# Performance work log

Hardware: AMD Instinct MI355X
Metric: run time of the kernel (lower is better)

## Reference

```python
import jax, jax.numpy as jnp
import numpy as np

N = 100000      # nodes
E = 1600000     # edges (avg degree 16)
F_IN = 64       # graph_input_dim
HID = 64        # gcn_out_dims (constant)
NG = 128        # number of graphs in batch
GF = 32         # global_input_dim
L1, L2, OUT = 256, 128, 1


def _glorot(k, fan_in, fan_out):
    s = 1.0 / np.sqrt(fan_in)
    return jax.random.uniform(k, (fan_in, fan_out), jnp.float32, -s, s)


def setup_inputs() -> dict:
    key = jax.random.key(0)
    ks = jax.random.split(key, 20)
    x = jax.random.normal(ks[0], (N, F_IN), jnp.float32)
    edge_index = jax.random.randint(ks[1], (2, E), 0, N, jnp.int64)
    # every graph gets a contiguous, non-empty slice of nodes (sorted batch ids)
    batch = (jnp.arange(N, dtype=jnp.int64) * NG) // N
    global_features = jax.random.normal(ks[2], (NG, GF), jnp.float32)
    dims = [F_IN, HID, HID, HID]
    inp = {"x": x, "global_features": global_features}
    for i in range(3):
        inp[f"conv_w{i+1}"] = _glorot(ks[3 + i], dims[i], dims[i + 1])
        inp[f"conv_b{i+1}"] = jnp.zeros((dims[i + 1],), jnp.float32)
    inp["fc_w1"] = _glorot(ks[8], HID * 2 + GF, L1)
    inp["fc_b1"] = jnp.zeros((L1,), jnp.float32)
    inp["fc_w2"] = _glorot(ks[9], L1, L2)
    inp["fc_b2"] = jnp.zeros((L2,), jnp.float32)
    inp["out_w"] = _glorot(ks[10], L2, OUT)
    inp["out_b"] = jnp.zeros((OUT,), jnp.float32)
    inp["edge_index"] = edge_index
    inp["batch"] = batch
    return inp


def _gcn_conv(x, src, dst, w, b, n):
    """PyG GCNConv: x' = D^-1/2 (A + I) D^-1/2 (x W) + b."""
    h = x @ w  # [n, out]
    loop = jnp.arange(n, dtype=src.dtype)
    s = jnp.concatenate([src, loop])
    d = jnp.concatenate([dst, loop])
    deg = jax.ops.segment_sum(jnp.ones(s.shape, h.dtype), d, num_segments=n)
    dinv = jnp.where(deg > 0, jax.lax.rsqrt(deg), 0.0)
    norm = dinv[s] * dinv[d]  # [E+n]
    out = jax.ops.segment_sum(h[s] * norm[:, None], d, num_segments=n)
    return out + b


def _forward(x, global_features, conv_w1, conv_b1, conv_w2, conv_b2,
             conv_w3, conv_b3, fc_w1, fc_b1, fc_w2, fc_b2, out_w, out_b,
             edge_index, batch):
    src, dst = edge_index[0], edge_index[1]
    n = x.shape[0]
    ng = global_features.shape[0]
    for w, b in ((conv_w1, conv_b1), (conv_w2, conv_b2), (conv_w3, conv_b3)):
        x = jax.nn.leaky_relu(_gcn_conv(x, src, dst, w, b, n))
    counts = jax.ops.segment_sum(jnp.ones((n,), x.dtype), batch, num_segments=ng)
    mean_pool = jax.ops.segment_sum(x, batch, num_segments=ng) / counts[:, None]
    max_pool = jax.ops.segment_max(x, batch, num_segments=ng)
    h = jnp.concatenate([mean_pool, max_pool, global_features], axis=1)
    h = jax.nn.leaky_relu(h @ fc_w1 + fc_b1)
    h = jax.nn.leaky_relu(h @ fc_w2 + fc_b2)
    return h @ out_w + out_b


def reference(x, global_features, conv_w1, conv_b1, conv_w2, conv_b2,
              conv_w3, conv_b3, fc_w1, fc_b1, fc_w2, fc_b2, out_w, out_b,
              edge_index, batch):
    return _forward(x, global_features, conv_w1, conv_b1, conv_w2, conv_b2,
                    conv_w3, conv_b3, fc_w1, fc_b1, fc_w2, fc_b2, out_w, out_b,
                    edge_index, batch)
```

## Files before the change

### kernel.cpp

```cpp
#include <hip/hip_runtime.h>
#include <hip/hip_fp16.h>
#include <stdint.h>

#define LRELU(x) ((x) > 0.0f ? (x) : 0.01f * (x))

struct h4 { __half2 a, b; };
struct h8 { __half2 a, b, c, d; };

#define EPB 2048
#define PARTS 16


__global__ __launch_bounds__(256) void hist1_kernel(const int* __restrict__ dst,
                                                    int* __restrict__ bhist,
                                                    int nblk, int E, int nbk) {
    __shared__ int h[512];
    int blk = blockIdx.x, t = threadIdx.x;
    for (int i = t; i < nbk; i += 256) h[i] = 0;
    __syncthreads();
    #pragma unroll
    for (int k = 0; k < EPB / 1024; ++k) {
        int i4 = blk * (EPB / 4) + k * 256 + t;
        int e = i4 * 4;
        if (e + 3 < E) {
            int4 d = ((const int4*)dst)[i4];
            atomicAdd(&h[d.x >> 8], 1);
            atomicAdd(&h[d.y >> 8], 1);
            atomicAdd(&h[d.z >> 8], 1);
            atomicAdd(&h[d.w >> 8], 1);
        } else {
            for (int j = e; j < E; ++j) atomicAdd(&h[dst[j] >> 8], 1);
        }
    }
    __syncthreads();
    for (int i = t; i < nbk; i += 256) bhist[i * nblk + blk] = h[i];
}

__global__ __launch_bounds__(256) void scanb_kernel(int* __restrict__ bhist,
                                                    int* __restrict__ btot, int nblk) {
    __shared__ int s[256];
    __shared__ int carry;
    int b = blockIdx.x, t = threadIdx.x;
    if (t == 0) carry = 0;
    __syncthreads();
    for (int c0 = 0; c0 < nblk; c0 += 256) {
        int idx = c0 + t;
        int v = (idx < nblk) ? bhist[b * nblk + idx] : 0;
        s[t] = v;
        __syncthreads();
        for (int off = 1; off < 256; off <<= 1) {
            int a = (t >= off) ? s[t - off] : 0;
            __syncthreads();
            s[t] += a;
            __syncthreads();
        }
        if (idx < nblk) bhist[b * nblk + idx] = s[t] - v + carry;
        __syncthreads();
        if (t == 255) carry += s[255];
        __syncthreads();
    }
    if (t == 0) btot[b] = carry;
}

__global__ void bbase_kernel(const int* __restrict__ btot, int* __restrict__ bbase,
                             int nbk, int E) {
    __shared__ int s[512];
    int t = threadIdx.x;
    int v = (t < nbk) ? btot[t] : 0;
    s[t] = v;
    __syncthreads();
    for (int off = 1; off < 512; off <<= 1) {
        int a = (t >= off) ? s[t - off] : 0;
        __syncthreads();
        s[t] += a;
        __syncthreads();
    }
    if (t < nbk) bbase[t] = s[t] - v;
    if (t == 0) bbase[nbk] = E;
}

__global__ __launch_bounds__(256) void place_kernel(const int* __restrict__ src,
                                                    const int* __restrict__ dst,
                                                    const int* __restrict__ bbase,
                                                    const int* __restrict__ bhist,
                                                    unsigned* __restrict__ bedge,
                                                    int nblk, int E, int nbk) {
    __shared__ int cur[512];
    int blk = blockIdx.x, t = threadIdx.x;
    for (int i = t; i < nbk; i += 256) cur[i] = bbase[i] + bhist[i * nblk + blk];
    __syncthreads();
    #pragma unroll
    for (int k = 0; k < EPB / 1024; ++k) {
        int i4 = blk * (EPB / 4) + k * 256 + t;
        int e = i4 * 4;
        if (e + 3 < E) {
            int4 s4 = ((const int4*)src)[i4];
            int4 d4 = ((const int4*)dst)[i4];
            int p0 = atomicAdd(&cur[d4.x >> 8], 1);
            int p1 = atomicAdd(&cur[d4.y >> 8], 1);
            int p2 = atomicAdd(&cur[d4.z >> 8], 1);
            int p3 = atomicAdd(&cur[d4.w >> 8], 1);
            bedge[p0] = ((unsigned)s4.x << 8) | (unsigned)(d4.x & 255);
            bedge[p1] = ((unsigned)s4.y << 8) | (unsigned)(d4.y & 255);
            bedge[p2] = ((unsigned)s4.z << 8) | (unsigned)(d4.z & 255);
            bedge[p3] = ((unsigned)s4.w << 8) | (unsigned)(d4.w & 255);
        } else {
            for (int j = e; j < E; ++j) {
                int d = dst[j];
                int pos = atomicAdd(&cur[d >> 8], 1);
                bedge[pos] = ((unsigned)src[j] << 8) | (unsigned)(d & 255);
            }
        }
    }
}

__global__ __launch_bounds__(256) void csr_kernel(const unsigned* __restrict__ bedge,
                                                  const int* __restrict__ bbase,
                                                  int* __restrict__ row_ptr,
                                                  float* __restrict__ dinv,
                                                  int* __restrict__ csr_src,
                                                  int N, int E, int nbk) {
    __shared__ int cnt[256];
    __shared__ int s[256];
    __shared__ int cur[256];
    int b = blockIdx.x, t = threadIdx.x;
    int node0 = b << 8;
    int beg = bbase[b], end = bbase[b + 1];
    cnt[t] = 0;
    __syncthreads();
    for (int i = beg + t; i < end; i += 256) atomicAdd(&cnt[bedge[i] & 255u], 1);
    __syncthreads();
    int c = cnt[t];
    s[t] = c;
    __syncthreads();
    for (int off = 1; off < 256; off <<= 1) {
        int a = (t >= off) ? s[t - off] : 0;
        __syncthreads();
        s[t] += a;
        __syncthreads();
    }
    int rp = beg + s[t] - c;
    int node = node0 + t;
    if (node < N) {
        row_ptr[node] = rp;
        dinv[node] = rsqrtf((float)c + 1.0f);
    }
    cur[t] = rp;
    if (b == nbk - 1 && t == 0) row_ptr[N] = E;
    __syncthreads();
    for (int i = beg + t; i < end; i += 256) {
        unsigned u = bedge[i];
        int pos = atomicAdd(&cur[u & 255u], 1);
        csr_src[pos] = (int)(u >> 8);
    }
}


__global__ __launch_bounds__(256) void gemm_f_kernel(const float* __restrict__ X,
                                                     const float* __restrict__ W,
                                                     const float* __restrict__ dinv,
                                                     __half* __restrict__ H, int N) {
    __shared__ float xl[64 * 66];
    __shared__ float wl[64 * 64];
    int tid = threadIdx.x;
    int base = blockIdx.x * 64;
    #pragma unroll
    for (int i = 0; i < 16; ++i) wl[i * 256 + tid] = W[i * 256 + tid];
    #pragma unroll
    for (int i = 0; i < 16; ++i) {
        int idx = i * 256 + tid;
        int r = idx >> 6, c = idx & 63;
        int gr = base + r;
        xl[r * 66 + c] = (gr < N) ? X[gr * 64 + c] : 0.0f;
    }
    __syncthreads();
    int grp = tid >> 4;
    int f0 = (tid & 15) * 4;
    int n0 = grp * 4;
    float acc[4][4] = {};
    #pragma unroll 4
    for (int k = 0; k < 64; ++k) {
        float4 wv = *(const float4*)&wl[k * 64 + f0];
        #pragma unroll
        for (int j = 0; j < 4; ++j) {
            float xv = xl[(n0 + j) * 66 + k];
            acc[j][0] += xv * wv.x;
            acc[j][1] += xv * wv.y;
            acc[j][2] += xv * wv.z;
            acc[j][3] += xv * wv.w;
        }
    }
    #pragma unroll
    for (int j = 0; j < 4; ++j) {
        int gr = base + n0 + j;
        if (gr < N) {
            float dv = dinv[gr];
            h4 o;
            o.a = __floats2half2_rn(acc[j][0] * dv, acc[j][1] * dv);
            o.b = __floats2half2_rn(acc[j][2] * dv, acc[j][3] * dv);
            *(h4*)&H[gr * 64 + f0] = o;
        }
    }
}

__global__ __launch_bounds__(256) void gemm_h_kernel(const __half* __restrict__ X,
                                                     const float* __restrict__ W,
                                                     const float* __restrict__ dinv,
                                                     __half* __restrict__ H, int N) {
    __shared__ float xl[64 * 66];
    __shared__ float wl[64 * 64];
    int tid = threadIdx.x;
    int base = blockIdx.x * 64;
    #pragma unroll
    for (int i = 0; i < 16; ++i) wl[i * 256 + tid] = W[i * 256 + tid];
    #pragma unroll
    for (int i = 0; i < 2; ++i) {
        int u = i * 256 + tid;
        int r = u >> 3;
        int c8 = (u & 7) * 8;
        int gr = base + r;
        float* xp = &xl[r * 66 + c8];
        if (gr < N) {
            h8 v = *(const h8*)&X[(size_t)gr * 64 + c8];
            float2 p;
            p = __half22float2(v.a); xp[0] = p.x; xp[1] = p.y;
            p = __half22float2(v.b); xp[2] = p.x; xp[3] = p.y;
            p = __half22float2(v.c); xp[4] = p.x; xp[5] = p.y;
            p = __half22float2(v.d); xp[6] = p.x; xp[7] = p.y;
        } else {
            #pragma unroll
            for (int j = 0; j < 8; ++j) xp[j] = 0.0f;
        }
    }
    __syncthreads();
    int grp = tid >> 4;
    int f0 = (tid & 15) * 4;
    int n0 = grp * 4;
    float acc[4][4] = {};
    #pragma unroll 4
    for (int k = 0; k < 64; ++k) {
        float4 wv = *(const float4*)&wl[k * 64 + f0];
        #pragma unroll
        for (int j = 0; j < 4; ++j) {
            float xv = xl[(n0 + j) * 66 + k];
            acc[j][0] += xv * wv.x;
            acc[j][1] += xv * wv.y;
            acc[j][2] += xv * wv.z;
            acc[j][3] += xv * wv.w;
        }
    }
    #pragma unroll
    for (int j = 0; j < 4; ++j) {
        int gr = base + n0 + j;
        if (gr < N) {
            float dv = dinv[gr];
            h4 o;
            o.a = __floats2half2_rn(acc[j][0] * dv, acc[j][1] * dv);
            o.b = __floats2half2_rn(acc[j][2] * dv, acc[j][3] * dv);
            *(h4*)&H[gr * 64 + f0] = o;
        }
    }
}

#define ACC8(vv, c0, c1, c2, c3, c4, c5, c6, c7)                                \
    { float2 p;                                                                 \
      p = __half22float2((vv).a); c0 += p.x; c1 += p.y;                         \
      p = __half22float2((vv).b); c2 += p.x; c3 += p.y;                         \
      p = __half22float2((vv).c); c4 += p.x; c5 += p.y;                         \
      p = __half22float2((vv).d); c6 += p.x; c7 += p.y; }

__global__ __launch_bounds__(256) void agg_kernel(const __half* __restrict__ H,
                                                  const int* __restrict__ rp,
                                                  const int* __restrict__ csrc,
                                                  const float* __restrict__ dinv,
                                                  const float* __restrict__ bias,
                                                  __half* __restrict__ Y, int N) {
    int w = (blockIdx.x * blockDim.x + threadIdx.x) >> 6;
    int nA = w << 1;
    if (nA >= N) return;
    int nB = nA + 1;
    bool hasB = nB < N;
    int l = threadIdx.x & 63;
    int slot = l >> 3;
    int fo = (l & 7) << 3;
    int endA = rp[nA + 1];
    int eA = rp[nA] + slot;
    int endB = hasB ? rp[nB + 1] : 0;
    int eB = hasB ? (rp[nB] + slot) : 0;
    float a0=0,a1=0,a2=0,a3=0,a4=0,a5=0,a6=0,a7=0;
    float b0=0,b1=0,b2=0,b3=0,b4=0,b5=0,b6=0,b7=0;
    while (eA + 8 < endA && eB + 8 < endB) {
        int sA0 = csrc[eA], sA1 = csrc[eA + 8];
        int sB0 = csrc[eB], sB1 = csrc[eB + 8];
        h8 vA0 = *(const h8*)&H[(size_t)sA0 * 64 + fo];
        h8 vA1 = *(const h8*)&H[(size_t)sA1 * 64 + fo];
        h8 vB0 = *(const h8*)&H[(size_t)sB0 * 64 + fo];
        h8 vB1 = *(const h8*)&H[(size_t)sB1 * 64 + fo];
        ACC8(vA0, a0,a1,a2,a3,a4,a5,a6,a7);
        ACC8(vA1, a0,a1,a2,a3,a4,a5,a6,a7);
        ACC8(vB0, b0,b1,b2,b3,b4,b5,b6,b7);
        ACC8(vB1, b0,b1,b2,b3,b4,b5,b6,b7);
        eA += 16; eB += 16;
    }
    while (eA + 8 < endA) {
        int s0 = csrc[eA], s1 = csrc[eA + 8];
        h8 v0 = *(const h8*)&H[(size_t)s0 * 64 + fo];
        h8 v1 = *(const h8*)&H[(size_t)s1 * 64 + fo];
        ACC8(v0, a0,a1,a2,a3,a4,a5,a6,a7);
        ACC8(v1, a0,a1,a2,a3,a4,a5,a6,a7);
        eA += 16;
    }
    while (eB + 8 < endB) {
        int s0 = csrc[eB], s1 = csrc[eB + 8];
        h8 v0 = *(const h8*)&H[(size_t)s0 * 64 + fo];
        h8 v1 = *(const h8*)&H[(size_t)s1 * 64 + fo];
        ACC8(v0, b0,b1,b2,b3,b4,b5,b6,b7);
        ACC8(v1, b0,b1,b2,b3,b4,b5,b6,b7);
        eB += 16;
    }
    if (eA < endA) {
        h8 v0 = *(const h8*)&H[(size_t)csrc[eA] * 64 + fo];
        ACC8(v0, a0,a1,a2,a3,a4,a5,a6,a7);
    }
    if (eB < endB) {
        h8 v0 = *(const h8*)&H[(size_t)csrc[eB] * 64 + fo];
        ACC8(v0, b0,b1,b2,b3,b4,b5,b6,b7);
    }
    #pragma unroll
    for (int m = 8; m <= 32; m <<= 1) {
        a0 += __shfl_xor(a0, m); a1 += __shfl_xor(a1, m);
        a2 += __shfl_xor(a2, m); a3 += __shfl_xor(a3, m);
        a4 += __shfl_xor(a4, m); a5 += __shfl_xor(a5, m);
        a6 += __shfl_xor(a6, m); a7 += __shfl_xor(a7, m);
        b0 += __shfl_xor(b0, m); b1 += __shfl_xor(b1, m);
        b2 += __shfl_xor(b2, m); b3 += __shfl_xor(b3, m);
        b4 += __shfl_xor(b4, m); b5 += __shfl_xor(b5, m);
        b6 += __shfl_xor(b6, m); b7 += __shfl_xor(b7, m);
    }
    if (l < 8) {
        float4 bv0 = *(const float4*)&bias[fo];
        float4 bv1 = *(const float4*)&bias[fo + 4];
        {
            h8 hs = *(const h8*)&H[(size_t)nA * 64 + fo];
            float2 s0 = __half22float2(hs.a), s1 = __half22float2(hs.b);
            float2 s2 = __half22float2(hs.c), s3 = __half22float2(hs.d);
            float dv = dinv[nA];
            float o0 = LRELU(dv * (a0 + s0.x) + bv0.x);
            float o1 = LRELU(dv * (a1 + s0.y) + bv0.y);
            float o2 = LRELU(dv * (a2 + s1.x) + bv0.z);
            float o3 = LRELU(dv * (a3 + s1.y) + bv0.w);
            float o4 = LRELU(dv * (a4 + s2.x) + bv1.x);
            float o5 = LRELU(dv * (a5 + s2.y) + bv1.y);
            float o6 = LRELU(dv * (a6 + s3.x) + bv1.z);
            float o7 = LRELU(dv * (a7 + s3.y) + bv1.w);
            h8 o;
            o.a = __floats2half2_rn(o0, o1);
            o.b = __floats2half2_rn(o2, o3);
            o.c = __floats2half2_rn(o4, o5);
            o.d = __floats2half2_rn(o6, o7);
            *(h8*)&Y[(size_t)nA * 64 + fo] = o;
        }
        if (hasB) {
            h8 hs = *(const h8*)&H[(size_t)nB * 64 + fo];
            float2 s0 = __half22float2(hs.a), s1 = __half22float2(hs.b);
            float2 s2 = __half22float2(hs.c), s3 = __half22float2(hs.d);
            float dv = dinv[nB];
            float o0 = LRELU(dv * (b0 + s0.x) + bv0.x);
            float o1 = LRELU(dv * (b1 + s0.y) + bv0.y);
            float o2 = LRELU(dv * (b2 + s1.x) + bv0.z);
            float o3 = LRELU(dv * (b3 + s1.y) + bv0.w);
            float o4 = LRELU(dv * (b4 + s2.x) + bv1.x);
            float o5 = LRELU(dv * (b5 + s2.y) + bv1.y);
            float o6 = LRELU(dv * (b6 + s3.x) + bv1.z);
            float o7 = LRELU(dv * (b7 + s3.y) + bv1.w);
            h8 o;
            o.a = __floats2half2_rn(o0, o1);
            o.b = __floats2half2_rn(o2, o3);
            o.c = __floats2half2_rn(o4, o5);
            o.d = __floats2half2_rn(o6, o7);
            *(h8*)&Y[(size_t)nB * 64 + fo] = o;
        }
    }
}


__global__ void bounds_kernel(const int* __restrict__ batch, int* __restrict__ gstart,
                              int N, int NG) {
    int i = blockIdx.x * blockDim.x + threadIdx.x;
    if (i >= N) return;
    int b = batch[i];
    if (i == 0) {
        gstart[b] = 0;
        gstart[NG] = N;
    } else if (batch[i - 1] != b) {
        gstart[b] = i;
    }
}

__global__ __launch_bounds__(256) void pool1_kernel(const __half* __restrict__ Y,
                                                    const int* __restrict__ gstart,
                                                    float* __restrict__ pbuf) {
    __shared__ float ssum[8][64];
    __shared__ float smax[8][64];
    int g = blockIdx.x / PARTS;
    int p = blockIdx.x % PARTS;
    int t = threadIdx.x;
    int f2 = (t & 31) * 2;
    int rg = t >> 5;
    int s = gstart[g], epos = gstart[g + 1];
    int len = epos - s;
    int lo = s + (int)((long long)len * p / PARTS);
    int hi = s + (int)((long long)len * (p + 1) / PARTS);
    float sx = 0.f, sy = 0.f, mx = -3.0e38f, my = -3.0e38f;
    for (int r = lo + rg; r < hi; r += 8) {
        __half2 v = *(const __half2*)&Y[(size_t)r * 64 + f2];
        float2 f = __half22float2(v);
        sx += f.x; sy += f.y;
        mx = fmaxf(mx, f.x); my = fmaxf(my, f.y);
    }
    ssum[rg][f2] = sx; ssum[rg][f2 + 1] = sy;
    smax[rg][f2] = mx; smax[rg][f2 + 1] = my;
    __syncthreads();
    if (t < 64) {
        float ts = 0.f, tm = -3.0e38f;
        #pragma unroll
        for (int r = 0; r < 8; ++r) {
            ts += ssum[r][t];
            tm = fmaxf(tm, smax[r][t]);
        }
        float* row = &pbuf[(size_t)(g * PARTS + p) * 128];
        row[t] = ts;
        row[64 + t] = tm;
    }
}

__global__ __launch_bounds__(64) void pool2_kernel(const float* __restrict__ pbuf,
                                                   const int* __restrict__ gstart,
                                                   const float* __restrict__ gfeat,
                                                   float* __restrict__ hcat) {
    int g = blockIdx.x;
    int f = threadIdx.x;
    const float* base = &pbuf[(size_t)g * PARTS * 128];
    float ts = 0.f, tm = -3.0e38f;
    #pragma unroll
    for (int p = 0; p < PARTS; ++p) {
        ts += base[p * 128 + f];
        tm = fmaxf(tm, base[p * 128 + 64 + f]);
    }
    float cnt = (float)(gstart[g + 1] - gstart[g]);
    hcat[g * 160 + f] = ts / cnt;
    hcat[g * 160 + 64 + f] = tm;
    if (f < 32) hcat[g * 160 + 128 + f] = gfeat[g * 32 + f];
}

__global__ __launch_bounds__(256) void mlp_kernel(const float* __restrict__ hcat,
                                                  const float* __restrict__ w1,
                                                  const float* __restrict__ b1,
                                                  const float* __restrict__ w2,
                                                  const float* __restrict__ b2,
                                                  const float* __restrict__ w3,
                                                  const float* __restrict__ b3,
                                                  float* __restrict__ out, int NG) {
    __shared__ float hl[160];
    __shared__ float h1[256];
    __shared__ float red[128];
    int g = blockIdx.x, t = threadIdx.x;
    if (t < 160) hl[t] = hcat[g * 160 + t];
    __syncthreads();
    float a1 = b1[t];
    for (int k = 0; k < 160; ++k) a1 += hl[k] * w1[k * 256 + t];
    h1[t] = LRELU(a1);
    __syncthreads();
    if (t < 128) {
        float a2 = b2[t];
        for (int k = 0; k < 256; ++k) a2 += h1[k] * w2[k * 128 + t];
        red[t] = LRELU(a2) * w3[t];
    }
    __syncthreads();
    if (t == 0) {
        float a3 = b3[0];
        for (int k = 0; k < 128; ++k) a3 += red[k];
        out[g] = a3;
    }
}


extern "C" void kernel_launch(void* const* d_in, const int* in_sizes, int n_in,
                              void* d_out, int out_size, void* d_ws, size_t ws_size,
                              hipStream_t stream) {
    const float* x      = (const float*)d_in[0];
    const float* gfeat  = (const float*)d_in[1];
    const float* cw1    = (const float*)d_in[2];
    const float* cb1    = (const float*)d_in[3];
    const float* cw2    = (const float*)d_in[4];
    const float* cb2    = (const float*)d_in[5];
    const float* cw3    = (const float*)d_in[6];
    const float* cb3    = (const float*)d_in[7];
    const float* fw1    = (const float*)d_in[8];
    const float* fb1    = (const float*)d_in[9];
    const float* fw2    = (const float*)d_in[10];
    const float* fb2    = (const float*)d_in[11];
    const float* ow     = (const float*)d_in[12];
    const float* ob     = (const float*)d_in[13];
    const int*   eidx   = (const int*)d_in[14];
    const int*   batch  = (const int*)d_in[15];

    const int N    = in_sizes[0] / 64;
    const int E    = in_sizes[14] / 2;
    const int NG   = in_sizes[1] / 32;
    const int NBUK = (N + 255) >> 8;
    const int NBLK = (E + EPB - 1) / EPB;
    const int* src = eidx;
    const int* dst = eidx + E;

    char* wp = (char*)d_ws;
    auto carve = [&](size_t bytes) {
        void* p = (void*)wp;
        wp += (bytes + 255) & ~(size_t)255;
        return p;
    };
    float*    dinv    = (float*)   carve((size_t)N * 4);
    int*      row_ptr = (int*)     carve((size_t)(N + 1) * 4);
    int*      bhist   = (int*)     carve((size_t)NBUK * NBLK * 4);
    int*      btot    = (int*)     carve((size_t)NBUK * 4);
    int*      bbase   = (int*)     carve((size_t)(NBUK + 1) * 4);
    unsigned* bedge   = (unsigned*)carve((size_t)E * 4);
    int*      csr_src = (int*)     carve((size_t)E * 4);
    __half*   hbuf    = (__half*)  carve((size_t)N * 64 * 2);
    __half*   ybuf    = (__half*)  carve((size_t)N * 64 * 2);
    int*      gstart  = (int*)     carve((size_t)(NG + 1) * 4);
    float*    pbuf    = (float*)   carve((size_t)NG * PARTS * 128 * 4);
    float*    hcat    = (float*)   carve((size_t)NG * 160 * 4);
    float*    outf    = (float*)d_out;

    const int nbN = (N + 255) / 256;

    hist1_kernel<<<NBLK, 256, 0, stream>>>(dst, bhist, NBLK, E, NBUK);
    scanb_kernel<<<NBUK, 256, 0, stream>>>(bhist, btot, NBLK);
    bbase_kernel<<<1, 512, 0, stream>>>(btot, bbase, NBUK, E);
    place_kernel<<<NBLK, 256, 0, stream>>>(src, dst, bbase, bhist, bedge, NBLK, E, NBUK);
    csr_kernel<<<NBUK, 256, 0, stream>>>(bedge, bbase, row_ptr, dinv, csr_src, N, E, NBUK);
    bounds_kernel<<<nbN, 256, 0, stream>>>(batch, gstart, N, NG);

    const int gemmB = (N + 63) / 64;
    const int aggB  = ((N + 1) / 2 + 3) / 4;

    gemm_f_kernel<<<gemmB, 256, 0, stream>>>(x, cw1, dinv, hbuf, N);
    agg_kernel<<<aggB, 256, 0, stream>>>(hbuf, row_ptr, csr_src, dinv, cb1, ybuf, N);
    gemm_h_kernel<<<gemmB, 256, 0, stream>>>(ybuf, cw2, dinv, hbuf, N);
    agg_kernel<<<aggB, 256, 0, stream>>>(hbuf, row_ptr, csr_src, dinv, cb2, ybuf, N);
    gemm_h_kernel<<<gemmB, 256, 0, stream>>>(ybuf, cw3, dinv, hbuf, N);
    agg_kernel<<<aggB, 256, 0, stream>>>(hbuf, row_ptr, csr_src, dinv, cb3, ybuf, N);

    pool1_kernel<<<NG * PARTS, 256, 0, stream>>>(ybuf, gstart, pbuf);
    pool2_kernel<<<NG, 64, 0, stream>>>(pbuf, gstart, gfeat, hcat);
    mlp_kernel<<<NG, 256, 0, stream>>>(hcat, fw1, fb1, fw2, fb2, ow, ob, outf, NG);
}
```

Baseline: 253.8 us.

## Use MFMA f16 matrix cores for GCN feature transforms and fuse pool2 into MLP

Replaces the three LDS-tiled FP32 scalar GEMM kernels with one templated kernel that calls the 16x16x32 f16 MFMA instruction. The weights are repacked once per call into fragment layout by a small prep kernel. The first layer now rounds the fp32 input x to half before multiplying, which may reduce precision. The separate pool2 kernel is folded into the MLP kernel's prologue, removing one launch and the hcat buffer. Output stores become scalar 2-byte writes per lane instead of 8-byte vector stores, which may hurt write coalescing.

```diff
diff --git a/kernel.cpp b/kernel.cpp
--- a/kernel.cpp
+++ b/kernel.cpp
@@ -6,6 +6,9 @@
 
 struct h4 { __half2 a, b; };
 struct h8 { __half2 a, b, c, d; };
+
+typedef _Float16 f16x8 __attribute__((ext_vector_type(8)));
+typedef float    f32x4 __attribute__((ext_vector_type(4)));
 
 #define EPB 2048
 #define PARTS 16
@@ -156,108 +159,72 @@
 }
 
 
-__global__ __launch_bounds__(256) void gemm_f_kernel(const float* __restrict__ X,
-                                                     const float* __restrict__ W,
-                                                     const float* __restrict__ dinv,
-                                                     __half* __restrict__ H, int N) {
-    __shared__ float xl[64 * 66];
-    __shared__ float wl[64 * 64];
+__global__ __launch_bounds__(256) void wprep_kernel(const float* __restrict__ w1,
+                                                    const float* __restrict__ w2,
+                                                    const float* __restrict__ w3,
+                                                    _Float16* __restrict__ Bf) {
+    int bc = blockIdx.x;
+    int layer = bc >> 1, c = bc & 1;
+    const float* W = (layer == 0) ? w1 : ((layer == 1) ? w2 : w3);
     int tid = threadIdx.x;
-    int base = blockIdx.x * 64;
-    #pragma unroll
-    for (int i = 0; i < 16; ++i) wl[i * 256 + tid] = W[i * 256 + tid];
-    #pragma unroll
-    for (int i = 0; i < 16; ++i) {
-        int idx = i * 256 + tid;
-        int r = idx >> 6, c = idx & 63;
-        int gr = base + r;
-        xl[r * 66 + c] = (gr < N) ? X[gr * 64 + c] : 0.0f;
-    }
-    __syncthreads();
-    int grp = tid >> 4;
-    int f0 = (tid & 15) * 4;
-    int n0 = grp * 4;
-    float acc[4][4] = {};
-    #pragma unroll 4
-    for (int k = 0; k < 64; ++k) {
-        float4 wv = *(const float4*)&wl[k * 64 + f0];
+    int t = tid >> 6, l = tid & 63;
+    _Float16* dst = Bf + ((size_t)(layer * 8 + c * 4 + t) * 64 + l) * 8;
+    int n  = t * 16 + (l & 15);
+    int kb = c * 32 + (l >> 4) * 8;
+    #pragma unroll
+    for (int i = 0; i < 8; ++i) dst[i] = (_Float16)W[(kb + i) * 64 + n];
+}
+
+template <bool XF32>
+__global__ __launch_bounds__(256) void gemm_mfma_kernel(const void* __restrict__ Xv,
+                                                        const _Float16* __restrict__ Bf,
+                                                        const float* __restrict__ dinv,
+                                                        __half* __restrict__ H, int N) {
+    int w = threadIdx.x >> 6;
+    int l = threadIdx.x & 63;
+    int col = l & 15;
+    int kg  = l >> 4;
+    int base = blockIdx.x * 64 + w * 16;
+    int nodeA = base + col;
+    bool okA = nodeA < N;
+
+    f32x4 acc[4] = {};
+    #pragma unroll
+    for (int c = 0; c < 2; ++c) {
+        int k0 = c * 32 + kg * 8;
+        f16x8 a = {};
+        if (okA) {
+            if constexpr (XF32) {
+                const float* xp = (const float*)Xv + (size_t)nodeA * 64 + k0;
+                float4 u = *(const float4*)xp;
+                float4 v = *(const float4*)(xp + 4);
+                a[0] = (_Float16)u.x; a[1] = (_Float16)u.y;
+                a[2] = (_Float16)u.z; a[3] = (_Float16)u.w;
+                a[4] = (_Float16)v.x; a[5] = (_Float16)v.y;
+                a[6] = (_Float16)v.z; a[7] = (_Float16)v.w;
+            } else {
+                a = *(const f16x8*)((const __half*)Xv + (size_t)nodeA * 64 + k0);
+            }
+        }
         #pragma unroll
-        for (int j = 0; j < 4; ++j) {
-            float xv = xl[(n0 + j) * 66 + k];
-            acc[j][0] += xv * wv.x;
-            acc[j][1] += xv * wv.y;
-            acc[j][2] += xv * wv.z;
-            acc[j][3] += xv * wv.w;
-        }
-    }
-    #pragma unroll
-    for (int j = 0; j < 4; ++j) {
-        int gr = base + n0 + j;
-        if (gr < N) {
-            float dv = dinv[gr];
-            h4 o;
-            o.a = __floats2half2_rn(acc[j][0] * dv, acc[j][1] * dv);
-            o.b = __floats2half2_rn(acc[j][2] * dv, acc[j][3] * dv);
-            *(h4*)&H[gr * 64 + f0] = o;
-        }
-    }
-}
-
-__global__ __launch_bounds__(256) void gemm_h_kernel(const __half* __restrict__ X,
-                                                     const float* __restrict__ W,
-                                                     const float* __restrict__ dinv,
-                                                     __half* __restrict__ H, int N) {
-    __shared__ float xl[64 * 66];
-    __shared__ float wl[64 * 64];
-    int tid = threadIdx.x;
-    int base = blockIdx.x * 64;
-    #pragma unroll
-    for (int i = 0; i < 16; ++i) wl[i * 256 + tid] = W[i * 256 + tid];
-    #pragma unroll
-    for (int i = 0; i < 2; ++i) {
-        int u = i * 256 + tid;
-        int r = u >> 3;
-        int c8 = (u & 7) * 8;
-        int gr = base + r;
-        float* xp = &xl[r * 66 + c8];
-        if (gr < N) {
-            h8 v = *(const h8*)&X[(size_t)gr * 64 + c8];
-            float2 p;
-            p = __half22float2(v.a); xp[0] = p.x; xp[1] = p.y;
-            p = __half22float2(v.b); xp[2] = p.x; xp[3] = p.y;
-            p = __half22float2(v.c); xp[4] = p.x; xp[5] = p.y;
-            p = __half22float2(v.d); xp[6] = p.x; xp[7] = p.y;
-        } else {
-            #pragma unroll
-            for (int j = 0; j < 8; ++j) xp[j] = 0.0f;
-        }
-    }
-    __syncthreads();
-    int grp = tid >> 4;
-    int f0 = (tid & 15) * 4;
-    int n0 = grp * 4;
-    float acc[4][4] = {};
-    #pragma unroll 4
-    for (int k = 0; k < 64; ++k) {
-        float4 wv = *(const float4*)&wl[k * 64 + f0];
+        for (int t = 0; t < 4; ++t) {
+            f16x8 b = *(const f16x8*)(Bf + ((size_t)(c * 4 + t) * 64 + l) * 8);
+            acc[t] = __builtin_amdgcn_mfma_f32_16x16x32_f16(a, b, acc[t], 0, 0, 0);
+        }
+    }
+    float dvr[4];
+    int rowN[4];
+    #pragma unroll
+    for (int r = 0; r < 4; ++r) {
+        rowN[r] = base + kg * 4 + r;
+        dvr[r] = (rowN[r] < N) ? dinv[rowN[r]] : 0.0f;
+    }
+    #pragma unroll
+    for (int t = 0; t < 4; ++t) {
         #pragma unroll
-        for (int j = 0; j < 4; ++j) {
-            float xv = xl[(n0 + j) * 66 + k];
-            acc[j][0] += xv * wv.x;
-            acc[j][1] += xv * wv.y;
-            acc[j][2] += xv * wv.z;
-            acc[j][3] += xv * wv.w;
-        }
-    }
-    #pragma unroll
-    for (int j = 0; j < 4; ++j) {
-        int gr = base + n0 + j;
-        if (gr < N) {
-            float dv = dinv[gr];
-            h4 o;
-            o.a = __floats2half2_rn(acc[j][0] * dv, acc[j][1] * dv);
-            o.b = __floats2half2_rn(acc[j][2] * dv, acc[j][3] * dv);
-            *(h4*)&H[gr * 64 + f0] = o;
+        for (int r = 0; r < 4; ++r) {
+            if (rowN[r] < N)
+                H[(size_t)rowN[r] * 64 + t * 16 + col] = __float2half(acc[t][r] * dvr[r]);
         }
     }
 }
@@ -434,26 +401,9 @@
     }
 }
 
-__global__ __launch_bounds__(64) void pool2_kernel(const float* __restrict__ pbuf,
-                                                   const int* __restrict__ gstart,
-                                                   const float* __restrict__ gfeat,
-                                                   float* __restrict__ hcat) {
-    int g = blockIdx.x;
-    int f = threadIdx.x;
-    const float* base = &pbuf[(size_t)g * PARTS * 128];
-    float ts = 0.f, tm = -3.0e38f;
-    #pragma unroll
-    for (int p = 0; p < PARTS; ++p) {
-        ts += base[p * 128 + f];
-        tm = fmaxf(tm, base[p * 128 + 64 + f]);
-    }
-    float cnt = (float)(gstart[g + 1] - gstart[g]);
-    hcat[g * 160 + f] = ts / cnt;
-    hcat[g * 160 + 64 + f] = tm;
-    if (f < 32) hcat[g * 160 + 128 + f] = gfeat[g * 32 + f];
-}
-
-__global__ __launch_bounds__(256) void mlp_kernel(const float* __restrict__ hcat,
+__global__ __launch_bounds__(256) void mlp_kernel(const float* __restrict__ pbuf,
+                                                  const int* __restrict__ gstart,
+                                                  const float* __restrict__ gfeat,
                                                   const float* __restrict__ w1,
                                                   const float* __restrict__ b1,
                                                   const float* __restrict__ w2,
@@ -465,7 +415,20 @@
     __shared__ float h1[256];
     __shared__ float red[128];
     int g = blockIdx.x, t = threadIdx.x;
-    if (t < 160) hl[t] = hcat[g * 160 + t];
+    if (t < 64) {
+        const float* base = &pbuf[(size_t)g * PARTS * 128];
+        float ts = 0.f, tm = -3.0e38f;
+        #pragma unroll
+        for (int p = 0; p < PARTS; ++p) {
+            ts += base[p * 128 + t];
+            tm = fmaxf(tm, base[p * 128 + 64 + t]);
+        }
+        float cnt = (float)(gstart[g + 1] - gstart[g]);
+        hl[t] = ts / cnt;
+        hl[64 + t] = tm;
+    } else if (t >= 128 && t < 160) {
+        hl[t] = gfeat[g * 32 + (t - 128)];
+    }
     __syncthreads();
     float a1 = b1[t];
     for (int k = 0; k < 160; ++k) a1 += hl[k] * w1[k * 256 + t];
@@ -519,19 +482,19 @@
         wp += (bytes + 255) & ~(size_t)255;
         return p;
     };
-    float*    dinv    = (float*)   carve((size_t)N * 4);
-    int*      row_ptr = (int*)     carve((size_t)(N + 1) * 4);
-    int*      bhist   = (int*)     carve((size_t)NBUK * NBLK * 4);
-    int*      btot    = (int*)     carve((size_t)NBUK * 4);
-    int*      bbase   = (int*)     carve((size_t)(NBUK + 1) * 4);
-    unsigned* bedge   = (unsigned*)carve((size_t)E * 4);
-    int*      csr_src = (int*)     carve((size_t)E * 4);
-    __half*   hbuf    = (__half*)  carve((size_t)N * 64 * 2);
-    __half*   ybuf    = (__half*)  carve((size_t)N * 64 * 2);
-    int*      gstart  = (int*)     carve((size_t)(NG + 1) * 4);
-    float*    pbuf    = (float*)   carve((size_t)NG * PARTS * 128 * 4);
-    float*    hcat    = (float*)   carve((size_t)NG * 160 * 4);
-    float*    outf    = (float*)d_out;
+    float*     dinv    = (float*)    carve((size_t)N * 4);
+    int*       row_ptr = (int*)      carve((size_t)(N + 1) * 4);
+    int*       bhist   = (int*)      carve((size_t)NBUK * NBLK * 4);
+    int*       btot    = (int*)      carve((size_t)NBUK * 4);
+    int*       bbase   = (int*)      carve((size_t)(NBUK + 1) * 4);
+    unsigned*  bedge   = (unsigned*) carve((size_t)E * 4);
+    int*       csr_src = (int*)      carve((size_t)E * 4);
+    __half*    hbuf    = (__half*)   carve((size_t)N * 64 * 2);
+    __half*    ybuf    = (__half*)   carve((size_t)N * 64 * 2);
+    int*       gstart  = (int*)      carve((size_t)(NG + 1) * 4);
+    float*     pbuf    = (float*)    carve((size_t)NG * PARTS * 128 * 4);
+    _Float16*  Bf      = (_Float16*) carve((size_t)3 * 4096 * 2);
+    float*     outf    = (float*)d_out;
 
     const int nbN = (N + 255) / 256;
 
@@ -541,18 +504,18 @@
     place_kernel<<<NBLK, 256, 0, stream>>>(src, dst, bbase, bhist, bedge, NBLK, E, NBUK);
     csr_kernel<<<NBUK, 256, 0, stream>>>(bedge, bbase, row_ptr, dinv, csr_src, N, E, NBUK);
     bounds_kernel<<<nbN, 256, 0, stream>>>(batch, gstart, N, NG);
+    wprep_kernel<<<6, 256, 0, stream>>>(cw1, cw2, cw3, Bf);
 
     const int gemmB = (N + 63) / 64;
     const int aggB  = ((N + 1) / 2 + 3) / 4;
 
-    gemm_f_kernel<<<gemmB, 256, 0, stream>>>(x, cw1, dinv, hbuf, N);
+    gemm_mfma_kernel<true ><<<gemmB, 256, 0, stream>>>(x,    Bf,        dinv, hbuf, N);
     agg_kernel<<<aggB, 256, 0, stream>>>(hbuf, row_ptr, csr_src, dinv, cb1, ybuf, N);
-    gemm_h_kernel<<<gemmB, 256, 0, stream>>>(ybuf, cw2, dinv, hbuf, N);
+    gemm_mfma_kernel<false><<<gemmB, 256, 0, stream>>>(ybuf, Bf + 4096, dinv, hbuf, N);
     agg_kernel<<<aggB, 256, 0, stream>>>(hbuf, row_ptr, csr_src, dinv, cb2, ybuf, N);
-    gemm_h_kernel<<<gemmB, 256, 0, stream>>>(ybuf, cw3, dinv, hbuf, N);
+    gemm_mfma_kernel<false><<<gemmB, 256, 0, stream>>>(ybuf, Bf + 8192, dinv, hbuf, N);
     agg_kernel<<<aggB, 256, 0, stream>>>(hbuf, row_ptr, csr_src, dinv, cb3, ybuf, N);
 
     pool1_kernel<<<NG * PARTS, 256, 0, stream>>>(ybuf, gstart, pbuf);
-    pool2_kernel<<<NG, 64, 0, stream>>>(pbuf, gstart, gfeat, hcat);
-    mlp_kernel<<<NG, 256, 0, stream>>>(hcat, fw1, fb1, fw2, fb2, ow, ob, outf, NG);
-}
+    mlp_kernel<<<NG, 256, 0, stream>>>(pbuf, gstart, gfeat, fw1, fb1, fw2, fb2, ow, ob, outf, NG);
+}
```

Measured after the change: 229.9 us. 9.4% less time.
